# Performance work log

Measured on AMD Instinct MI355X. Metric: run time of the kernel, lower is better.

Reference implementation:

```python
import jax, jax.numpy as jnp
import numpy as np

B, N, D_IN, D_OUT = 16, 2048, 128, 128

def setup_inputs() -> dict:
    key = jax.random.key(0)
    ks = jax.random.split(key, 8)
    x = jax.random.normal(ks[0], (B, N, D_IN), dtype=jnp.float32)
    adj = jax.random.randint(ks[1], (N, N), 0, 2).astype(jnp.float32)
    # Conv1d(kernel_size=1) weights, PyTorch default uniform init scale
    s_emb = 1.0 / np.sqrt(D_IN)
    W_emb = jax.random.uniform(ks[2], (D_OUT, D_IN), jnp.float32, -s_emb, s_emb)
    b_emb = jax.random.uniform(ks[3], (D_OUT,), jnp.float32, -s_emb, s_emb)
    s_qk = 1.0 / np.sqrt(D_OUT)
    w_q = jax.random.uniform(ks[4], (D_OUT,), jnp.float32, -s_qk, s_qk)
    b_q = jax.random.uniform(ks[5], (1,), jnp.float32, -s_qk, s_qk)
    w_k = jax.random.uniform(ks[6], (D_OUT,), jnp.float32, -s_qk, s_qk)
    b_k = jax.random.uniform(ks[7], (1,), jnp.float32, -s_qk, s_qk)
    return {"x": x, "adj": adj, "W_emb": W_emb, "b_emb": b_emb,
            "w_q": w_q, "b_q": b_q, "w_k": w_k, "b_k": b_k}

def reference(x, adj, W_emb, b_emb, w_q, b_q, w_k, b_k):
    # emb_conv: 1x1 conv over node dim == per-node linear  [B,N,D_out]
    seq_fts = jnp.einsum('bni,oi->bno', x, W_emb) + b_emb
    # q_conv / k_conv: project to scalar per node  [B,N]
    q = jnp.einsum('bnd,d->bn', seq_fts, w_q) + b_q  # f_1_t squeezed
    k = jnp.einsum('bnd,d->bn', seq_fts, w_k) + b_k  # f_2_t squeezed
    # f[b,i,j] = f_1_t[b,0,j] + f_2_t^T[b,i,0] = q[b,j] + k[b,i]
    f = k[:, :, None] + q[:, None, :]                 # [B,N,N]
    f = jax.nn.leaky_relu(adj[None, :, :] * f, negative_slope=0.01)
    coefs = jax.nn.softmax(f, axis=1)                 # softmax over dim=1 (rows)
    vals = jnp.einsum('bij,bjd->bid', coefs, seq_fts)  # [B,N,D_out]
    return vals
```

## Files before the change

### kernel.cpp

```cpp
#include <hip/hip_runtime.h>
#include <hip/hip_bf16.h>
#include <stdint.h>

#define B_ 16
#define N_ 2048
#define D_ 128

typedef __bf16 bf16_t;
typedef bf16_t bf16x8 __attribute__((ext_vector_type(8)));
typedef float f32x4 __attribute__((ext_vector_type(4)));

__global__ __launch_bounds__(256, 2) void k_emb(const float* __restrict__ x,
                                                const float* __restrict__ W,
                                                const float* __restrict__ be,
                                                const float* __restrict__ wq,
                                                const float* __restrict__ bq,
                                                const float* __restrict__ wk,
                                                const float* __restrict__ bk,
                                                const float* __restrict__ adj,
                                                unsigned int* __restrict__ bits,
                                                bf16_t* __restrict__ Pb,
                                                float* __restrict__ qa, float* __restrict__ ka,
                                                float* __restrict__ Eq, float* __restrict__ eqs,
                                                float* __restrict__ Ek, float* __restrict__ eks) {
    __shared__ float xs[32][68];
    __shared__ float ws[32][132];
    __shared__ float qs[64], ks[64];
    int b  = blockIdx.y;
    int n0 = blockIdx.x * 64;
    int tid = threadIdx.x;
    int tx = tid & 15, ty = tid >> 4;
    if (tid < 64) { qs[tid] = 0.f; ks[tid] = 0.f; }

    {
        int base = (blockIdx.y * (N_ / 64) + blockIdx.x) * 256 + tid;
#pragma unroll 8
        for (int it = 0; it < (N_ * N_) / (512 * 256); ++it) {
            int t = base + it * (512 * 256);
            float v = adj[t];
            unsigned long long m = __ballot(v > 0.5f);
            if ((t & 63) == 0) {
                int i = t >> 11;
                int j = t & 2047;
                bits[i * 64 + (j >> 5)]     = (unsigned int)m;
                bits[i * 64 + (j >> 5) + 1] = (unsigned int)(m >> 32);
            }
        }
    }

    float acc[4][8] = {};
    f32x4 xr[2], wr[4];

    auto loadregs = [&](int kc) {
#pragma unroll
        for (int s = 0; s < 2; ++s) {
            int p = tid + 256 * s;
            int n = p >> 3, kq = p & 7;
            xr[s] = *(const f32x4*)(x + ((size_t)(b * N_ + n0 + n)) * D_ + kc * 32 + kq * 4);
        }
#pragma unroll
        for (int s = 0; s < 4; ++s) {
            int p = tid + 256 * s;
            int d = p >> 3, kq = p & 7;
            wr[s] = *(const f32x4*)(W + (size_t)d * D_ + kc * 32 + kq * 4);
        }
    };
    auto writelds = [&]() {
#pragma unroll
        for (int s = 0; s < 2; ++s) {
            int p = tid + 256 * s;
            int n = p >> 3, kq = p & 7;
#pragma unroll
            for (int u = 0; u < 4; ++u) xs[kq * 4 + u][n] = xr[s][u];
        }
#pragma unroll
        for (int s = 0; s < 4; ++s) {
            int p = tid + 256 * s;
            int d = p >> 3, kq = p & 7;
#pragma unroll
            for (int u = 0; u < 4; ++u) ws[kq * 4 + u][d] = wr[s][u];
        }
    };

    loadregs(0);
    for (int kc = 0; kc < 4; ++kc) {
        writelds();
        __syncthreads();
        if (kc < 3) loadregs(kc + 1);
#pragma unroll 4
        for (int k = 0; k < 32; ++k) {
            f32x4 xv  = *(const f32x4*)&xs[k][tx * 4];
            f32x4 wv0 = *(const f32x4*)&ws[k][ty * 8];
            f32x4 wv1 = *(const f32x4*)&ws[k][ty * 8 + 4];
#pragma unroll
            for (int i = 0; i < 4; ++i)
#pragma unroll
                for (int j = 0; j < 8; ++j)
                    acc[i][j] += xv[i] * ((j < 4) ? wv0[j] : wv1[j - 4]);
        }
        __syncthreads();
    }

    float qp[4] = {}, kp[4] = {};
#pragma unroll
    for (int j = 0; j < 8; ++j) {
        int d = ty * 8 + j;
        float bj  = be[d];
        float wqj = wq[d];
        float wkj = wk[d];
        f32x4 o;
        bf16_t ob[4];
#pragma unroll
        for (int i = 0; i < 4; ++i) {
            o[i] = acc[i][j] + bj;
            qp[i] += o[i] * wqj;
            kp[i] += o[i] * wkj;
            ob[i] = (bf16_t)o[i];
        }
        *(uint2*)(Pb + ((size_t)b * D_ + d) * N_ + n0 + tx * 4) = *(uint2*)ob;
    }
#pragma unroll
    for (int i = 0; i < 4; ++i) {
        atomicAdd(&qs[tx * 4 + i], qp[i]);
        atomicAdd(&ks[tx * 4 + i], kp[i]);
    }
    __syncthreads();
    if (tid < 64) {
        int idx = b * N_ + n0 + tid;
        float aq = qs[tid] + bq[0];
        float ak = ks[tid] + bk[0];
        qa[idx] = aq;          ka[idx] = ak;
        Eq[idx] = expf(aq);    eqs[idx] = expf(0.01f * aq);
        Ek[idx] = expf(ak);    eks[idx] = expf(0.01f * ak);
    }
}

__global__ __launch_bounds__(1024) void k_denom(const unsigned int* __restrict__ bits,
                                                const float* __restrict__ qa,
                                                const float* __restrict__ ka,
                                                const float* __restrict__ Eq,
                                                const float* __restrict__ eqs,
                                                const float* __restrict__ Ek,
                                                const float* __restrict__ eks,
                                                float* __restrict__ rd,
                                                float* __restrict__ Eqr,
                                                float* __restrict__ eqr) {
    __shared__ float red[8][128];
    int jt  = blockIdx.x;
    int b   = blockIdx.y;
    int tid = threadIdx.x;
    int tj  = tid & 127;
    int sg  = tid >> 7;
    int j   = jt * 128 + tj;
    float qj  = qa[b * N_ + j];
    float Eqj = Eq[b * N_ + j];
    float eqj = eqs[b * N_ + j];
    int shift = j & 31;
    int wid   = j >> 5;
    float acc = 0.f;
    int i0 = sg * 256;
#pragma unroll 16
    for (int i = i0; i < i0 + 256; ++i) {
        float kk  = ka[b * N_ + i];
        float Ekk = Ek[b * N_ + i];
        float ekk = eks[b * N_ + i];
        unsigned int w = bits[i * 64 + wid];
        float z  = kk + qj;
        float f1 = z > 0.f ? Ekk : ekk;
        float f2 = z > 0.f ? Eqj : eqj;
        acc += ((w >> shift) & 1u) ? f1 * f2 : 1.0f;
    }
    red[sg][tj] = acc;
    __syncthreads();
    if (sg == 0) {
        float den = acc;
#pragma unroll
        for (int s = 1; s < 8; ++s) den += red[s][tj];
        float r = 1.0f / den;
        int idx = b * N_ + j;
        rd[idx]  = r;
        Eqr[idx] = Eqj * r;
        eqr[idx] = eqj * r;
    }
}

__global__ __launch_bounds__(256, 2) void k_attn(const float* __restrict__ qa,
                                                 const float* __restrict__ ka,
                                                 const float* __restrict__ Ek,
                                                 const float* __restrict__ eks,
                                                 const float* __restrict__ rd,
                                                 const float* __restrict__ Eqr,
                                                 const float* __restrict__ eqr,
                                                 const unsigned int* __restrict__ bits,
                                                 const bf16_t* __restrict__ Pb,
                                                 float* __restrict__ out) {
    __shared__ __align__(16) bf16_t ldsB[2][128 * 64];
    __shared__ __align__(16) bf16_t ldsA[4 * 2 * 64 * 8];
    int n     = blockIdx.x;
    int xcd   = n & 7;
    int slot  = n >> 3;
    int b     = xcd * 2 + (slot >> 5);
    int ibase = (slot & 31) * 64;
    int tid   = threadIdx.x;
    int w     = tid >> 6;
    int lane  = tid & 63;
    int m16   = lane & 15;
    int quad  = lane >> 4;
    int ig    = w & 1;
    int dg    = w >> 1;

    int iA = ibase + (2 * ig) * 16 + m16;
    int iB = iA + 16;
    float mkR0 = -ka[b * N_ + iA], mkR1 = -ka[b * N_ + iB];
    float EkR0 = Ek[b * N_ + iA],  EkR1 = Ek[b * N_ + iB];
    float ekR0 = eks[b * N_ + iA], ekR1 = eks[b * N_ + iB];
    const unsigned int* brA = bits + (size_t)iA * 64;
    const unsigned int* brB = bits + (size_t)iB * 64;
    const float* qp  = qa  + b * N_;
    const float* Erp = Eqr + b * N_;
    const float* erp = eqr + b * N_;
    const float* rdp = rd  + b * N_;
    const bf16_t* PtB = Pb + (size_t)b * D_ * N_;

    f32x4 acc[2][4];
#pragma unroll
    for (int c = 0; c < 2; ++c)
#pragma unroll
        for (int nt = 0; nt < 4; ++nt) acc[c][nt] = (f32x4){0.f, 0.f, 0.f, 0.f};

    f32x4 qv4[2][2], Er4[2][2], er4[2][2], rd4[2][2];
    unsigned int mA[2], mB[2];

    auto ldj = [&](int par, int jb) {
        int j0 = jb + dg * 32 + quad * 8;
        qv4[par][0] = *(const f32x4*)(qp  + j0);
        qv4[par][1] = *(const f32x4*)(qp  + j0 + 4);
        Er4[par][0] = *(const f32x4*)(Erp + j0);
        Er4[par][1] = *(const f32x4*)(Erp + j0 + 4);
        er4[par][0] = *(const f32x4*)(erp + j0);
        er4[par][1] = *(const f32x4*)(erp + j0 + 4);
        rd4[par][0] = *(const f32x4*)(rdp + j0);
        rd4[par][1] = *(const f32x4*)(rdp + j0 + 4);
        mA[par] = brA[(jb >> 5) + dg];
        mB[par] = brB[(jb >> 5) + dg];
    };

    auto stage = [&](int bufi, int jb) {
#pragma unroll
        for (int t = 0; t < 4; ++t) {
            int off = t * 4096 + tid * 16;
            int d   = off >> 7;
            int g   = ((off & 127) >> 4) ^ (d & 7);
            const bf16_t* gp = PtB + (size_t)d * N_ + jb + g * 8;
            __builtin_amdgcn_global_load_lds(
                (const __attribute__((address_space(1))) void*)gp,
                (__attribute__((address_space(3))) void*)((char*)(&ldsB[bufi][0]) + off),
                16, 0, 0);
        }
    };

    auto agen = [&](int par, bf16x8& afA, bf16x8& afB) {
#pragma unroll
        for (int t = 0; t < 8; ++t) {
            float qv = (t < 4) ? qv4[par][0][t] : qv4[par][1][t - 4];
            float Er = (t < 4) ? Er4[par][0][t] : Er4[par][1][t - 4];
            float er = (t < 4) ? er4[par][0][t] : er4[par][1][t - 4];
            float rj = (t < 4) ? rd4[par][0][t] : rd4[par][1][t - 4];
            int bit = quad * 8 + t;
            {
                bool c = qv > mkR0;
                float v = (c ? EkR0 : ekR0) * (c ? Er : er);
                afA[t] = (bf16_t)(((mA[par] >> bit) & 1u) ? v : rj);
            }
            {
                bool c = qv > mkR1;
                float v = (c ? EkR1 : ekR1) * (c ? Er : er);
                afB[t] = (bf16_t)(((mB[par] >> bit) & 1u) ? v : rj);
            }
        }
        *(bf16x8*)((char*)ldsA + ((((2 * ig + 0) * 2 + dg) * 64 + lane) * 16)) = afA;
        *(bf16x8*)((char*)ldsA + ((((2 * ig + 1) * 2 + dg) * 64 + lane) * 16)) = afB;
    };

    auto mfma_phase = [&](int buf, const bf16x8& afA, const bf16x8& afB) {
        {
            int cph = ((dg * 4 + quad) ^ (m16 & 7)) * 8;
#pragma unroll
            for (int nt = 0; nt < 4; ++nt) {
                int d = dg * 64 + nt * 16 + m16;
                bf16x8 bf = *(const bf16x8*)&ldsB[buf][d * 64 + cph];
                acc[0][nt] = __builtin_amdgcn_mfma_f32_16x16x32_bf16(afA, bf, acc[0][nt], 0, 0, 0);
                acc[1][nt] = __builtin_amdgcn_mfma_f32_16x16x32_bf16(afB, bf, acc[1][nt], 0, 0, 0);
            }
        }
        {
            int oh = 1 - dg;
            bf16x8 a0 = *(const bf16x8*)((char*)ldsA + ((((2 * ig + 0) * 2 + oh) * 64 + lane) * 16));
            bf16x8 a1 = *(const bf16x8*)((char*)ldsA + ((((2 * ig + 1) * 2 + oh) * 64 + lane) * 16));
            int cph = ((oh * 4 + quad) ^ (m16 & 7)) * 8;
#pragma unroll
            for (int nt = 0; nt < 4; ++nt) {
                int d = dg * 64 + nt * 16 + m16;
                bf16x8 bf = *(const bf16x8*)&ldsB[buf][d * 64 + cph];
                acc[0][nt] = __builtin_amdgcn_mfma_f32_16x16x32_bf16(a0, bf, acc[0][nt], 0, 0, 0);
                acc[1][nt] = __builtin_amdgcn_mfma_f32_16x16x32_bf16(a1, bf, acc[1][nt], 0, 0, 0);
            }
        }
    };

    stage(0, 0);
    ldj(0, 0);
    int buf = 0;
#pragma unroll 1
    for (int s2 = 0; s2 < 15; ++s2) {
#pragma unroll
        for (int par = 0; par < 2; ++par) {
            int jb = (s2 * 2 + par) * 64;
            ldj(par ^ 1, jb + 64);
            stage(buf ^ 1, jb + 64);

            bf16x8 afA, afB;
            agen(par, afA, afB);
            asm volatile("s_waitcnt vmcnt(14) lgkmcnt(0)" ::: "memory");
            __builtin_amdgcn_s_barrier();

            __builtin_amdgcn_s_setprio(1);
            mfma_phase(buf, afA, afB);
            __builtin_amdgcn_s_setprio(0);

            asm volatile("s_waitcnt lgkmcnt(0)" ::: "memory");
            __builtin_amdgcn_s_barrier();
            buf ^= 1;
        }
    }
    {
        ldj(1, 31 * 64);
        stage(buf ^ 1, 31 * 64);
        bf16x8 afA, afB;
        agen(0, afA, afB);
        asm volatile("s_waitcnt vmcnt(14) lgkmcnt(0)" ::: "memory");
        __builtin_amdgcn_s_barrier();
        __builtin_amdgcn_s_setprio(1);
        mfma_phase(buf, afA, afB);
        __builtin_amdgcn_s_setprio(0);
        asm volatile("s_waitcnt lgkmcnt(0)" ::: "memory");
        __builtin_amdgcn_s_barrier();
        buf ^= 1;
    }
    {
        bf16x8 afA, afB;
        agen(1, afA, afB);
        asm volatile("s_waitcnt vmcnt(0) lgkmcnt(0)" ::: "memory");
        __builtin_amdgcn_s_barrier();
        __builtin_amdgcn_s_setprio(1);
        mfma_phase(buf, afA, afB);
        __builtin_amdgcn_s_setprio(0);
    }

#pragma unroll
    for (int c = 0; c < 2; ++c) {
        int irow = ibase + (2 * ig + c) * 16 + quad * 4;
#pragma unroll
        for (int nt = 0; nt < 4; ++nt) {
            int d = dg * 64 + nt * 16 + m16;
#pragma unroll
            for (int r = 0; r < 4; ++r)
                out[((size_t)b * N_ + irow + r) * D_ + d] = acc[c][nt][r];
        }
    }
}

extern "C" void kernel_launch(void* const* d_in, const int* in_sizes, int n_in,
                              void* d_out, int out_size, void* d_ws, size_t ws_size,
                              hipStream_t stream) {
    const float* x   = (const float*)d_in[0];
    const float* adj = (const float*)d_in[1];
    const float* W   = (const float*)d_in[2];
    const float* be  = (const float*)d_in[3];
    const float* wq  = (const float*)d_in[4];
    const float* bq  = (const float*)d_in[5];
    const float* wk  = (const float*)d_in[6];
    const float* bk  = (const float*)d_in[7];
    float* out = (float*)d_out;

    char* ws = (char*)d_ws;
    size_t off = 0;
    bf16_t* Pb = (bf16_t*)(ws + off); off += (size_t)B_ * D_ * N_ * 2;
    float* qa  = (float*)(ws + off);  off += (size_t)B_ * N_ * 4;
    float* ka  = (float*)(ws + off);  off += (size_t)B_ * N_ * 4;
    float* Eq  = (float*)(ws + off);  off += (size_t)B_ * N_ * 4;
    float* eqs = (float*)(ws + off);  off += (size_t)B_ * N_ * 4;
    float* Ek  = (float*)(ws + off);  off += (size_t)B_ * N_ * 4;
    float* eks = (float*)(ws + off);  off += (size_t)B_ * N_ * 4;
    float* rd  = (float*)(ws + off);  off += (size_t)B_ * N_ * 4;
    float* Eqr = (float*)(ws + off);  off += (size_t)B_ * N_ * 4;
    float* eqr = (float*)(ws + off);  off += (size_t)B_ * N_ * 4;
    unsigned int* bits = (unsigned int*)(ws + off); off += (size_t)N_ * 64 * 4;

    k_emb<<<dim3(N_ / 64, B_), 256, 0, stream>>>(x, W, be, wq, bq, wk, bk,
                                                 adj, bits,
                                                 Pb, qa, ka, Eq, eqs, Ek, eks);
    k_denom<<<dim3(16, 16), 1024, 0, stream>>>(bits, qa, ka, Eq, eqs, Ek, eks,
                                               rd, Eqr, eqr);
    k_attn<<<512, 256, 0, stream>>>(qa, ka, Ek, eks, rd, Eqr, eqr,
                                    bits, Pb, out);
}
```

Before: 188.7 us.

## Double the j-tile to 128 and spread A-fragment generation across all waves

The attention kernel now processes 128 j-columns per pipeline step instead of 64. Each wave generates the A (coefficient) fragments for all four 16-row groups over its own 32-column slice and shares them through LDS. Every wave then reads all four k-slices back for its MFMAs. This halves the number of barrier-separated iterations and spreads the agen work evenly across waves, at the cost of twice the LDS (64 KB for B plus 16 KB for A), a wider XOR swizzle, and more registers for the per-row mask words.

```diff
diff --git a/kernel.cpp b/kernel.cpp
--- a/kernel.cpp
+++ b/kernel.cpp
@@ -194,8 +194,8 @@
                                                  const unsigned int* __restrict__ bits,
                                                  const bf16_t* __restrict__ Pb,
                                                  float* __restrict__ out) {
-    __shared__ __align__(16) bf16_t ldsB[2][128 * 64];
-    __shared__ __align__(16) bf16_t ldsA[4 * 2 * 64 * 8];
+    __shared__ __align__(16) bf16_t ldsB[2][128 * 128];
+    __shared__ __align__(16) bf16_t ldsA[4 * 4 * 64 * 8];
     int n     = blockIdx.x;
     int xcd   = n & 7;
     int slot  = n >> 3;
@@ -209,13 +209,16 @@
     int ig    = w & 1;
     int dg    = w >> 1;
 
-    int iA = ibase + (2 * ig) * 16 + m16;
-    int iB = iA + 16;
-    float mkR0 = -ka[b * N_ + iA], mkR1 = -ka[b * N_ + iB];
-    float EkR0 = Ek[b * N_ + iA],  EkR1 = Ek[b * N_ + iB];
-    float ekR0 = eks[b * N_ + iA], ekR1 = eks[b * N_ + iB];
-    const unsigned int* brA = bits + (size_t)iA * 64;
-    const unsigned int* brB = bits + (size_t)iB * 64;
+    float mkR[4], EkR[4], ekR[4];
+    const unsigned int* brC[4];
+#pragma unroll
+    for (int c = 0; c < 4; ++c) {
+        int ii = ibase + c * 16 + m16;
+        mkR[c] = -ka[b * N_ + ii];
+        EkR[c] = Ek[b * N_ + ii];
+        ekR[c] = eks[b * N_ + ii];
+        brC[c] = bits + (size_t)ii * 64;
+    }
     const float* qp  = qa  + b * N_;
     const float* Erp = Eqr + b * N_;
     const float* erp = eqr + b * N_;
@@ -229,10 +232,10 @@
         for (int nt = 0; nt < 4; ++nt) acc[c][nt] = (f32x4){0.f, 0.f, 0.f, 0.f};
 
     f32x4 qv4[2][2], Er4[2][2], er4[2][2], rd4[2][2];
-    unsigned int mA[2], mB[2];
+    unsigned int mK[2][4];
 
     auto ldj = [&](int par, int jb) {
-        int j0 = jb + dg * 32 + quad * 8;
+        int j0 = jb + w * 32 + quad * 8;
         qv4[par][0] = *(const f32x4*)(qp  + j0);
         qv4[par][1] = *(const f32x4*)(qp  + j0 + 4);
         Er4[par][0] = *(const f32x4*)(Erp + j0);
@@ -241,16 +244,17 @@
         er4[par][1] = *(const f32x4*)(erp + j0 + 4);
         rd4[par][0] = *(const f32x4*)(rdp + j0);
         rd4[par][1] = *(const f32x4*)(rdp + j0 + 4);
-        mA[par] = brA[(jb >> 5) + dg];
-        mB[par] = brB[(jb >> 5) + dg];
+        int wi = (jb >> 5) + w;
+#pragma unroll
+        for (int c = 0; c < 4; ++c) mK[par][c] = brC[c][wi];
     };
 
     auto stage = [&](int bufi, int jb) {
 #pragma unroll
-        for (int t = 0; t < 4; ++t) {
+        for (int t = 0; t < 8; ++t) {
             int off = t * 4096 + tid * 16;
-            int d   = off >> 7;
-            int g   = ((off & 127) >> 4) ^ (d & 7);
+            int d   = off >> 8;
+            int g   = ((off & 255) >> 4) ^ (d & 15);
             const bf16_t* gp = PtB + (size_t)d * N_ + jb + g * 8;
             __builtin_amdgcn_global_load_lds(
                 (const __attribute__((address_space(1))) void*)gp,
@@ -259,7 +263,8 @@
         }
     };
 
-    auto agen = [&](int par, bf16x8& afA, bf16x8& afB) {
+    auto agen = [&](int par) {
+        bf16x8 af[4];
 #pragma unroll
         for (int t = 0; t < 8; ++t) {
             float qv = (t < 4) ? qv4[par][0][t] : qv4[par][1][t - 4];
@@ -267,41 +272,28 @@
             float er = (t < 4) ? er4[par][0][t] : er4[par][1][t - 4];
             float rj = (t < 4) ? rd4[par][0][t] : rd4[par][1][t - 4];
             int bit = quad * 8 + t;
-            {
-                bool c = qv > mkR0;
-                float v = (c ? EkR0 : ekR0) * (c ? Er : er);
-                afA[t] = (bf16_t)(((mA[par] >> bit) & 1u) ? v : rj);
+#pragma unroll
+            for (int c = 0; c < 4; ++c) {
+                bool cc = qv > mkR[c];
+                float v = (cc ? EkR[c] : ekR[c]) * (cc ? Er : er);
+                af[c][t] = (bf16_t)(((mK[par][c] >> bit) & 1u) ? v : rj);
             }
-            {
-                bool c = qv > mkR1;
-                float v = (c ? EkR1 : ekR1) * (c ? Er : er);
-                afB[t] = (bf16_t)(((mB[par] >> bit) & 1u) ? v : rj);
-            }
-        }
-        *(bf16x8*)((char*)ldsA + ((((2 * ig + 0) * 2 + dg) * 64 + lane) * 16)) = afA;
-        *(bf16x8*)((char*)ldsA + ((((2 * ig + 1) * 2 + dg) * 64 + lane) * 16)) = afB;
-    };
-
-    auto mfma_phase = [&](int buf, const bf16x8& afA, const bf16x8& afB) {
-        {
-            int cph = ((dg * 4 + quad) ^ (m16 & 7)) * 8;
+        }
+#pragma unroll
+        for (int c = 0; c < 4; ++c)
+            *(bf16x8*)((char*)ldsA + (((c * 4 + w) * 64 + lane) * 16)) = af[c];
+    };
+
+    auto mfma_phase = [&](int buf) {
+#pragma unroll
+        for (int ks = 0; ks < 4; ++ks) {
+            bf16x8 a0 = *(const bf16x8*)((char*)ldsA + ((((2 * ig + 0) * 4 + ks) * 64 + lane) * 16));
+            bf16x8 a1 = *(const bf16x8*)((char*)ldsA + ((((2 * ig + 1) * 4 + ks) * 64 + lane) * 16));
+            int cph = ((ks * 4 + quad) ^ m16) * 8;
 #pragma unroll
             for (int nt = 0; nt < 4; ++nt) {
                 int d = dg * 64 + nt * 16 + m16;
-                bf16x8 bf = *(const bf16x8*)&ldsB[buf][d * 64 + cph];
-                acc[0][nt] = __builtin_amdgcn_mfma_f32_16x16x32_bf16(afA, bf, acc[0][nt], 0, 0, 0);
-                acc[1][nt] = __builtin_amdgcn_mfma_f32_16x16x32_bf16(afB, bf, acc[1][nt], 0, 0, 0);
-            }
-        }
-        {
-            int oh = 1 - dg;
-            bf16x8 a0 = *(const bf16x8*)((char*)ldsA + ((((2 * ig + 0) * 2 + oh) * 64 + lane) * 16));
-            bf16x8 a1 = *(const bf16x8*)((char*)ldsA + ((((2 * ig + 1) * 2 + oh) * 64 + lane) * 16));
-            int cph = ((oh * 4 + quad) ^ (m16 & 7)) * 8;
-#pragma unroll
-            for (int nt = 0; nt < 4; ++nt) {
-                int d = dg * 64 + nt * 16 + m16;
-                bf16x8 bf = *(const bf16x8*)&ldsB[buf][d * 64 + cph];
+                bf16x8 bf = *(const bf16x8*)&ldsB[buf][d * 128 + cph];
                 acc[0][nt] = __builtin_amdgcn_mfma_f32_16x16x32_bf16(a0, bf, acc[0][nt], 0, 0, 0);
                 acc[1][nt] = __builtin_amdgcn_mfma_f32_16x16x32_bf16(a1, bf, acc[1][nt], 0, 0, 0);
             }
@@ -312,20 +304,19 @@
     ldj(0, 0);
     int buf = 0;
 #pragma unroll 1
-    for (int s2 = 0; s2 < 15; ++s2) {
+    for (int s2 = 0; s2 < 7; ++s2) {
 #pragma unroll
         for (int par = 0; par < 2; ++par) {
-            int jb = (s2 * 2 + par) * 64;
-            ldj(par ^ 1, jb + 64);
-            stage(buf ^ 1, jb + 64);
-
-            bf16x8 afA, afB;
-            agen(par, afA, afB);
-            asm volatile("s_waitcnt vmcnt(14) lgkmcnt(0)" ::: "memory");
+            int jb = (s2 * 2 + par) * 128;
+            ldj(par ^ 1, jb + 128);
+            stage(buf ^ 1, jb + 128);
+
+            agen(par);
+            asm volatile("s_waitcnt vmcnt(20) lgkmcnt(0)" ::: "memory");
             __builtin_amdgcn_s_barrier();
 
             __builtin_amdgcn_s_setprio(1);
-            mfma_phase(buf, afA, afB);
+            mfma_phase(buf);
             __builtin_amdgcn_s_setprio(0);
 
             asm volatile("s_waitcnt lgkmcnt(0)" ::: "memory");
@@ -334,26 +325,24 @@
         }
     }
     {
-        ldj(1, 31 * 64);
-        stage(buf ^ 1, 31 * 64);
-        bf16x8 afA, afB;
-        agen(0, afA, afB);
-        asm volatile("s_waitcnt vmcnt(14) lgkmcnt(0)" ::: "memory");
+        ldj(1, 15 * 128);
+        stage(buf ^ 1, 15 * 128);
+        agen(0);
+        asm volatile("s_waitcnt vmcnt(20) lgkmcnt(0)" ::: "memory");
         __builtin_amdgcn_s_barrier();
         __builtin_amdgcn_s_setprio(1);
-        mfma_phase(buf, afA, afB);
+        mfma_phase(buf);
         __builtin_amdgcn_s_setprio(0);
         asm volatile("s_waitcnt lgkmcnt(0)" ::: "memory");
         __builtin_amdgcn_s_barrier();
         buf ^= 1;
     }
     {
-        bf16x8 afA, afB;
-        agen(1, afA, afB);
+        agen(1);
         asm volatile("s_waitcnt vmcnt(0) lgkmcnt(0)" ::: "memory");
         __builtin_amdgcn_s_barrier();
         __builtin_amdgcn_s_setprio(1);
-        mfma_phase(buf, afA, afB);
+        mfma_phase(buf);
         __builtin_amdgcn_s_setprio(0);
     }
 
```

New measurement: 192.2 us. About the same (+1.8%).

## Compute full A fragments per wave and drop LDS A exchange and barrier

Applied to the files above, without the earlier changes.

Each wave now generates the A-operand (attention coefficients) for both 32-column halves itself instead of splitting the work with the partner wave and exchanging it through LDS. Each wave also stages only its own d-half of the B tile, so the first barrier per step can be replaced by a per-wave vmcnt wait. This removes the LDS A round trip and one block barrier per iteration, at the cost of doubling the elementwise A-generation ALU work and the per-thread global loads and registers.

```diff
diff --git a/kernel.cpp b/kernel.cpp
--- a/kernel.cpp
+++ b/kernel.cpp
@@ -195,7 +195,6 @@
                                                  const bf16_t* __restrict__ Pb,
                                                  float* __restrict__ out) {
     __shared__ __align__(16) bf16_t ldsB[2][128 * 64];
-    __shared__ __align__(16) bf16_t ldsA[4 * 2 * 64 * 8];
     int n     = blockIdx.x;
     int xcd   = n & 7;
     int slot  = n >> 3;
@@ -228,30 +227,33 @@
 #pragma unroll
         for (int nt = 0; nt < 4; ++nt) acc[c][nt] = (f32x4){0.f, 0.f, 0.f, 0.f};
 
-    f32x4 qv4[2][2], Er4[2][2], er4[2][2], rd4[2][2];
-    unsigned int mA[2], mB[2];
+    f32x4 qv4[2][2][2], Er4[2][2][2], er4[2][2][2], rd4[2][2][2];
+    uint2 mAB[2][2];
 
     auto ldj = [&](int par, int jb) {
-        int j0 = jb + dg * 32 + quad * 8;
-        qv4[par][0] = *(const f32x4*)(qp  + j0);
-        qv4[par][1] = *(const f32x4*)(qp  + j0 + 4);
-        Er4[par][0] = *(const f32x4*)(Erp + j0);
-        Er4[par][1] = *(const f32x4*)(Erp + j0 + 4);
-        er4[par][0] = *(const f32x4*)(erp + j0);
-        er4[par][1] = *(const f32x4*)(erp + j0 + 4);
-        rd4[par][0] = *(const f32x4*)(rdp + j0);
-        rd4[par][1] = *(const f32x4*)(rdp + j0 + 4);
-        mA[par] = brA[(jb >> 5) + dg];
-        mB[par] = brB[(jb >> 5) + dg];
+#pragma unroll
+        for (int h = 0; h < 2; ++h) {
+            int j0 = jb + h * 32 + quad * 8;
+            qv4[par][h][0] = *(const f32x4*)(qp  + j0);
+            qv4[par][h][1] = *(const f32x4*)(qp  + j0 + 4);
+            Er4[par][h][0] = *(const f32x4*)(Erp + j0);
+            Er4[par][h][1] = *(const f32x4*)(Erp + j0 + 4);
+            er4[par][h][0] = *(const f32x4*)(erp + j0);
+            er4[par][h][1] = *(const f32x4*)(erp + j0 + 4);
+            rd4[par][h][0] = *(const f32x4*)(rdp + j0);
+            rd4[par][h][1] = *(const f32x4*)(rdp + j0 + 4);
+        }
+        mAB[par][0] = *(const uint2*)&brA[jb >> 5];
+        mAB[par][1] = *(const uint2*)&brB[jb >> 5];
     };
 
     auto stage = [&](int bufi, int jb) {
 #pragma unroll
-        for (int t = 0; t < 4; ++t) {
-            int off = t * 4096 + tid * 16;
-            int d   = off >> 7;
-            int g   = ((off & 127) >> 4) ^ (d & 7);
+        for (int t = 0; t < 8; ++t) {
+            int d   = dg * 64 + t * 8 + (lane >> 3);
+            int g   = (lane & 7) ^ (d & 7);
             const bf16_t* gp = PtB + (size_t)d * N_ + jb + g * 8;
+            int off = dg * 8192 + t * 1024 + lane * 16;
             __builtin_amdgcn_global_load_lds(
                 (const __attribute__((address_space(1))) void*)gp,
                 (__attribute__((address_space(3))) void*)((char*)(&ldsB[bufi][0]) + off),
@@ -259,51 +261,42 @@
         }
     };
 
-    auto agen = [&](int par, bf16x8& afA, bf16x8& afB) {
-#pragma unroll
-        for (int t = 0; t < 8; ++t) {
-            float qv = (t < 4) ? qv4[par][0][t] : qv4[par][1][t - 4];
-            float Er = (t < 4) ? Er4[par][0][t] : Er4[par][1][t - 4];
-            float er = (t < 4) ? er4[par][0][t] : er4[par][1][t - 4];
-            float rj = (t < 4) ? rd4[par][0][t] : rd4[par][1][t - 4];
-            int bit = quad * 8 + t;
-            {
-                bool c = qv > mkR0;
-                float v = (c ? EkR0 : ekR0) * (c ? Er : er);
-                afA[t] = (bf16_t)(((mA[par] >> bit) & 1u) ? v : rj);
+    auto agen = [&](int par, bf16x8 (&af)[2][2]) {
+#pragma unroll
+        for (int h = 0; h < 2; ++h) {
+            unsigned int mA = h ? mAB[par][0].y : mAB[par][0].x;
+            unsigned int mB = h ? mAB[par][1].y : mAB[par][1].x;
+#pragma unroll
+            for (int t = 0; t < 8; ++t) {
+                float qv = (t < 4) ? qv4[par][h][0][t] : qv4[par][h][1][t - 4];
+                float Er = (t < 4) ? Er4[par][h][0][t] : Er4[par][h][1][t - 4];
+                float er = (t < 4) ? er4[par][h][0][t] : er4[par][h][1][t - 4];
+                float rj = (t < 4) ? rd4[par][h][0][t] : rd4[par][h][1][t - 4];
+                int bit = quad * 8 + t;
+                {
+                    bool c = qv > mkR0;
+                    float v = (c ? EkR0 : ekR0) * (c ? Er : er);
+                    af[0][h][t] = (bf16_t)(((mA >> bit) & 1u) ? v : rj);
+                }
+                {
+                    bool c = qv > mkR1;
+                    float v = (c ? EkR1 : ekR1) * (c ? Er : er);
+                    af[1][h][t] = (bf16_t)(((mB >> bit) & 1u) ? v : rj);
+                }
             }
-            {
-                bool c = qv > mkR1;
-                float v = (c ? EkR1 : ekR1) * (c ? Er : er);
-                afB[t] = (bf16_t)(((mB[par] >> bit) & 1u) ? v : rj);
-            }
-        }
-        *(bf16x8*)((char*)ldsA + ((((2 * ig + 0) * 2 + dg) * 64 + lane) * 16)) = afA;
-        *(bf16x8*)((char*)ldsA + ((((2 * ig + 1) * 2 + dg) * 64 + lane) * 16)) = afB;
-    };
-
-    auto mfma_phase = [&](int buf, const bf16x8& afA, const bf16x8& afB) {
-        {
-            int cph = ((dg * 4 + quad) ^ (m16 & 7)) * 8;
+        }
+    };
+
+    auto mfma_phase = [&](int buf, bf16x8 (&af)[2][2]) {
+#pragma unroll
+        for (int h = 0; h < 2; ++h) {
+            int cph = ((h * 4 + quad) ^ (m16 & 7)) * 8;
 #pragma unroll
             for (int nt = 0; nt < 4; ++nt) {
                 int d = dg * 64 + nt * 16 + m16;
                 bf16x8 bf = *(const bf16x8*)&ldsB[buf][d * 64 + cph];
-                acc[0][nt] = __builtin_amdgcn_mfma_f32_16x16x32_bf16(afA, bf, acc[0][nt], 0, 0, 0);
-                acc[1][nt] = __builtin_amdgcn_mfma_f32_16x16x32_bf16(afB, bf, acc[1][nt], 0, 0, 0);
-            }
-        }
-        {
-            int oh = 1 - dg;
-            bf16x8 a0 = *(const bf16x8*)((char*)ldsA + ((((2 * ig + 0) * 2 + oh) * 64 + lane) * 16));
-            bf16x8 a1 = *(const bf16x8*)((char*)ldsA + ((((2 * ig + 1) * 2 + oh) * 64 + lane) * 16));
-            int cph = ((oh * 4 + quad) ^ (m16 & 7)) * 8;
-#pragma unroll
-            for (int nt = 0; nt < 4; ++nt) {
-                int d = dg * 64 + nt * 16 + m16;
-                bf16x8 bf = *(const bf16x8*)&ldsB[buf][d * 64 + cph];
-                acc[0][nt] = __builtin_amdgcn_mfma_f32_16x16x32_bf16(a0, bf, acc[0][nt], 0, 0, 0);
-                acc[1][nt] = __builtin_amdgcn_mfma_f32_16x16x32_bf16(a1, bf, acc[1][nt], 0, 0, 0);
+                acc[0][nt] = __builtin_amdgcn_mfma_f32_16x16x32_bf16(af[0][h], bf, acc[0][nt], 0, 0, 0);
+                acc[1][nt] = __builtin_amdgcn_mfma_f32_16x16x32_bf16(af[1][h], bf, acc[1][nt], 0, 0, 0);
             }
         }
     };
@@ -319,13 +312,12 @@
             ldj(par ^ 1, jb + 64);
             stage(buf ^ 1, jb + 64);
 
-            bf16x8 afA, afB;
-            agen(par, afA, afB);
-            asm volatile("s_waitcnt vmcnt(14) lgkmcnt(0)" ::: "memory");
-            __builtin_amdgcn_s_barrier();
+            bf16x8 af[2][2];
+            agen(par, af);
+            asm volatile("s_waitcnt vmcnt(26)" ::: "memory");
 
             __builtin_amdgcn_s_setprio(1);
-            mfma_phase(buf, afA, afB);
+            mfma_phase(buf, af);
             __builtin_amdgcn_s_setprio(0);
 
             asm volatile("s_waitcnt lgkmcnt(0)" ::: "memory");
@@ -336,24 +328,22 @@
     {
         ldj(1, 31 * 64);
         stage(buf ^ 1, 31 * 64);
-        bf16x8 afA, afB;
-        agen(0, afA, afB);
-        asm volatile("s_waitcnt vmcnt(14) lgkmcnt(0)" ::: "memory");
-        __builtin_amdgcn_s_barrier();
+        bf16x8 af[2][2];
+        agen(0, af);
+        asm volatile("s_waitcnt vmcnt(26)" ::: "memory");
         __builtin_amdgcn_s_setprio(1);
-        mfma_phase(buf, afA, afB);
+        mfma_phase(buf, af);
         __builtin_amdgcn_s_setprio(0);
         asm volatile("s_waitcnt lgkmcnt(0)" ::: "memory");
         __builtin_amdgcn_s_barrier();
         buf ^= 1;
     }
     {
-        bf16x8 afA, afB;
-        agen(1, afA, afB);
-        asm volatile("s_waitcnt vmcnt(0) lgkmcnt(0)" ::: "memory");
-        __builtin_amdgcn_s_barrier();
+        bf16x8 af[2][2];
+        agen(1, af);
+        asm volatile("s_waitcnt vmcnt(0)" ::: "memory");
         __builtin_amdgcn_s_setprio(1);
-        mfma_phase(buf, afA, afB);
+        mfma_phase(buf, af);
         __builtin_amdgcn_s_setprio(0);
     }
 
```

Result: slower. 217.8 us (+15.4%).
